# Kernel optimization log

Measured on AMD Instinct MI355X. Metric: run time of the kernel, lower is better.

Reference implementation:

```python
import jax, jax.numpy as jnp
import numpy as np

IN, H, L, S = 512, 512, 2, 3   # input_size, hidden_size, num_layers, num_split
B, T = 64, 512
PENALTY = 0.7                  # forward() default penalty arg


def gru_cell(x, h, Wih, Whh, bih, bhh):
    # torch.nn.GRUCell math, gate order (r, z, n)
    gi = x @ Wih.T + bih
    gh = h @ Whh.T + bhh
    ir, iz, inew = jnp.split(gi, 3, axis=-1)
    hr, hz, hn = jnp.split(gh, 3, axis=-1)
    r = jax.nn.sigmoid(ir + hr)
    z = jax.nn.sigmoid(iz + hz)
    n = jnp.tanh(inew + r * hn)
    return (1.0 - z) * n + z * h


def setup_inputs() -> dict:
    key = jax.random.key(0)
    ks = jax.random.split(key, 10)
    sc = 1.0 / np.sqrt(H)
    u = lambda k, shp: jax.random.uniform(k, shp, jnp.float32, -sc, sc)
    return {
        'x': jax.random.normal(ks[0], (B, T, IN), jnp.float32),
        'Wih_first': u(ks[1], (S, 3 * H, IN)),      # layer-0 input weights per expert
        'Wih_rest': u(ks[2], (S, L - 1, 3 * H, H)),  # layers 1..L-1 input weights per expert
        'Whh': u(ks[3], (S, L, 3 * H, H)),
        'bih': u(ks[4], (S, L, 3 * H)),
        'bhh': u(ks[5], (S, L, 3 * H)),
        'Wlw': u(ks[6], (H, H)),      # layer_weights Linear(H, H)
        'blw': u(ks[7], (H,)),
        'Wsel': u(ks[8], (S, H + IN)),  # selective_layer Linear(H+IN, S)
        'bsel': u(ks[9], (S,)),
    }


def _run_stack(x_t, h_prev, cur, Wih_first, Wih_rest, Whh, bih, bhh):
    # h_prev: [B, L, H]; cur: expert index (traced int ok)
    hs = [gru_cell(x_t, h_prev[:, 0], Wih_first[cur], Whh[cur, 0], bih[cur, 0], bhh[cur, 0])]
    for j in range(1, L):
        hs.append(gru_cell(hs[-1], h_prev[:, j], Wih_rest[cur, j - 1], Whh[cur, j], bih[cur, j], bhh[cur, j]))
    return jnp.stack(hs, axis=1)  # [B, L, H]


def _forward(x, Wih_first, Wih_rest, Whh, bih, bhh, Wlw, blw, Wsel, bsel):
    h0 = jnp.zeros((B, L, H), x.dtype)
    # timestep 0: hard-coded expert 0 on zero hidden
    h = _run_stack(x[:, 0], h0, 0, Wih_first, Wih_rest, Whh, bih, bhh)
    p = jnp.ones((S,), x.dtype).at[0].mul(PENALTY)
    p = p / p.max()

    def step(carry, x_t):
        h_prev, p = carry
        # attention-style router (num_layers > 1 branch of the original)
        energy = jnp.einsum('blh,gh->blg', h_prev, Wlw) + blw   # [B, L, H]
        le = energy.sum(-1)                                     # [B, L]
        sh = jnp.einsum('bl,blh->bh', le, h_prev)               # [B, H]
        logits = jnp.concatenate([sh, x_t], axis=-1) @ Wsel.T + bsel  # [B, S]
        probs = jax.nn.softmax(logits.sum(0)) * p               # [S]
        cur = jnp.argmax(probs)                                 # top-1 expert
        h_new = _run_stack(x_t, h_prev, cur, Wih_first, Wih_rest, Whh, bih, bhh)
        p_new = p * jnp.where(jnp.arange(S) == cur, PENALTY, 1.0)
        p_new = p_new / p_new.max()
        return (h_new, p_new), h_new[:, -1]

    (h_last, _), outs = jax.lax.scan(step, (h, p), jnp.swapaxes(x, 0, 1)[1:])
    outputs = jnp.concatenate([h[:, -1][None], outs], axis=0)   # [T, B, H]
    return outputs, h_last[:, -1]


def reference(x, Wih_first, Wih_rest, Whh, bih, bhh, Wlw, blw, Wsel, bsel):
    return _forward(x, Wih_first, Wih_rest, Whh, bih, bhh, Wlw, blw, Wsel, bsel)
```

## Files before the change

### kernel.cpp

```cpp
#include <hip/hip_runtime.h>
#include <math.h>

#define BB 64
#define TT 512
#define HH 512
#define KK 512
#define G3 1536
#define PEN 0.7f
#define NBLK 256
#define NTHR 512
#define SLAB 32768
#define WSTRIDE ((size_t)(G3 * KK))

__device__ __forceinline__ float4 ldcv4(const float* p) {
  float4 r;
  asm volatile("global_load_dwordx4 %0, %1, off sc0 sc1" : "=v"(r) : "v"(p));
  return r;
}
__device__ __forceinline__ void ld1_issue(float* dst, const float* p) {
  asm volatile("global_load_dword %0, %1, off sc0 sc1" : "=v"(*dst) : "v"(p));
}
__device__ __forceinline__ void stwt1(float* p, float v) {
  asm volatile("global_store_dword %0, %1, off sc0 sc1" :: "v"(p), "v"(v) : "memory");
}
__device__ __forceinline__ void vwait() {
  asm volatile("s_waitcnt vmcnt(0)" ::: "memory");
  __builtin_amdgcn_sched_barrier(0);
}
__device__ __forceinline__ unsigned umin2(unsigned a, unsigned b) { return a < b ? a : b; }
__device__ __forceinline__ void st_flag(unsigned* p, unsigned v) {
  __hip_atomic_store(p, v, __ATOMIC_RELAXED, __HIP_MEMORY_SCOPE_AGENT);
}
__device__ __forceinline__ void poll_all(const unsigned* flags, unsigned ep) {
  const unsigned* p = flags + (threadIdx.x & 63) * 4;
  for (;;) {
    uint4 v;
    asm volatile("global_load_dwordx4 %0, %1, off sc0 sc1" : "=v"(v) : "v"(p));
    vwait();
    unsigned mn = umin2(umin2(v.x, v.y), umin2(v.z, v.w));
    if (__all((int)(mn >= ep))) break;
    __builtin_amdgcn_s_sleep(2);
  }
}
__device__ __forceinline__ void poll8(const unsigned* flag8, unsigned ep) {
  const unsigned* p = flag8 + (threadIdx.x & 7);
  for (;;) {
    unsigned v;
    asm volatile("global_load_dword %0, %1, off sc0 sc1" : "=v"(v) : "v"(p));
    vwait();
    if (__all((int)(v >= ep))) break;
    __builtin_amdgcn_s_sleep(2);
  }
}

__global__ void k_pre_xc(const float* __restrict__ x, const float* __restrict__ Wsel,
                         const float* __restrict__ bsel, float* __restrict__ xc) {
  int t = blockIdx.x, tid = threadIdx.x;
  __shared__ float xs[512];
  __shared__ float a0[256], a1[256], a2[256];
  for (int i = tid; i < 512; i += 256) {
    float s = 0.f;
    const float* px = x + (size_t)t * KK + i;
    for (int b = 0; b < BB; ++b) s += px[(size_t)b * TT * KK];
    xs[i] = s;
  }
  __syncthreads();
  float c0 = 0.f, c1 = 0.f, c2 = 0.f;
  for (int i = tid; i < 512; i += 256) {
    float v = xs[i];
    c0 += v * Wsel[512 + i];
    c1 += v * Wsel[1024 + 512 + i];
    c2 += v * Wsel[2048 + 512 + i];
  }
  a0[tid] = c0; a1[tid] = c1; a2[tid] = c2;
  __syncthreads();
  for (int off = 128; off; off >>= 1) {
    if (tid < off) { a0[tid] += a0[tid + off]; a1[tid] += a1[tid + off]; a2[tid] += a2[tid + off]; }
    __syncthreads();
  }
  if (tid == 0) {
    xc[t * 4 + 0] = a0[0] + 64.f * bsel[0];
    xc[t * 4 + 1] = a1[0] + 64.f * bsel[1];
    xc[t * 4 + 2] = a2[0] + 64.f * bsel[2];
  }
}

__global__ void k_pre_misc(const float* __restrict__ Wlw, const float* __restrict__ blw,
                           const float* __restrict__ x,
                           float* __restrict__ wsum, float* __restrict__ bsumb,
                           float* __restrict__ xT0,
                           float* __restrict__ h0T0, float* __restrict__ h1T0,
                           unsigned* __restrict__ flags, unsigned* __restrict__ flag8) {
  int gtid = blockIdx.x * 256 + threadIdx.x;
  for (int i = gtid; i < SLAB; i += 64 * 256) { h0T0[i] = 0.f; h1T0[i] = 0.f; }
  for (int i = gtid; i < SLAB; i += 64 * 256) {
    int b = i >> 9, k = i & 511;
    xT0[(k >> 2) * 256 + b * 4 + (k & 3)] = x[(size_t)b * TT * KK + k];
  }
  if (blockIdx.x == 0) {
    int tid = threadIdx.x;
    if (tid < 256) flags[tid] = 0u;
    if (tid < 8) flag8[tid] = 0u;
    for (int h = tid; h < 512; h += 256) {
      float s = 0.f;
      for (int g = 0; g < 512; ++g) s += Wlw[(size_t)g * 512 + h];
      wsum[h] = s;
    }
    __shared__ float red[256];
    float s = 0.f;
    for (int i = tid; i < 512; i += 256) s += blw[i];
    red[tid] = s;
    __syncthreads();
    for (int off = 128; off; off >>= 1) {
      if (tid < off) red[tid] += red[tid + off];
      __syncthreads();
    }
    if (tid == 0) *bsumb = red[0];
  }
}

__global__ void k_pre_xt(const float* __restrict__ x, float* __restrict__ xTall) {
  int t = blockIdx.x, tid = threadIdx.x;
  float* dst = xTall + (size_t)t * SLAB;
  const float* src = x + (size_t)t * KK;
  for (int i = tid; i < SLAB; i += 256) {
    int b = i >> 9, k = i & 511;
    dst[(k >> 2) * 256 + b * 4 + (k & 3)] = src[(size_t)b * TT * KK + k];
  }
}

template<int ACT_CACHED>
__device__ __forceinline__ void do_layer(
    int tid, int b, int k0, int j0, int lidx, int bid,
    const float* __restrict__ act, const float* __restrict__ hT,
    const float* __restrict__ Wih, const float* __restrict__ Whh,
    const float* __restrict__ bihL, const float* __restrict__ bhhL,
    const float* __restrict__ wsum, const float* __restrict__ Wsel,
    float* __restrict__ houtT, float* __restrict__ houtN, float* __restrict__ houtN2,
    float* __restrict__ part, float* red, float* r2) {
  int w = tid >> 6;
  const float* a4p = act + (k0 >> 2) * 256 + b * 4;
  const float* h4p = hT + (k0 >> 2) * 256 + b * 4;
  const float* wi0r = Wih + (size_t)(j0 + 0) * KK + k0;
  const float* wi1r = Wih + (size_t)(j0 + 1) * KK + k0;
  const float* wi0z = Wih + (size_t)(512 + j0 + 0) * KK + k0;
  const float* wi1z = Wih + (size_t)(512 + j0 + 1) * KK + k0;
  const float* wi0n = Wih + (size_t)(1024 + j0 + 0) * KK + k0;
  const float* wi1n = Wih + (size_t)(1024 + j0 + 1) * KK + k0;
  const float* wh0r = Whh + (size_t)(j0 + 0) * KK + k0;
  const float* wh1r = Whh + (size_t)(j0 + 1) * KK + k0;
  const float* wh0z = Whh + (size_t)(512 + j0 + 0) * KK + k0;
  const float* wh1z = Whh + (size_t)(512 + j0 + 1) * KK + k0;
  const float* wh0n = Whh + (size_t)(1024 + j0 + 0) * KK + k0;
  const float* wh1n = Whh + (size_t)(1024 + j0 + 1) * KK + k0;
  float ai0r = 0.f, ai1r = 0.f, ai0z = 0.f, ai1z = 0.f, ai0n = 0.f, ai1n = 0.f;
  float ah0r = 0.f, ah1r = 0.f, ah0z = 0.f, ah1z = 0.f, ah0n = 0.f, ah1n = 0.f;
  float4 A[8], Hv[8];
  for (int half = 0; half < 2; ++half) {
    const float* ab = a4p + half * 2048;
    const float* hb = h4p + half * 2048;
#pragma unroll
    for (int i = 0; i < 8; ++i) {
      if (ACT_CACHED) A[i] = *(const float4*)(ab + i * 256);
      else            A[i] = ldcv4(ab + i * 256);
      Hv[i] = ldcv4(hb + i * 256);
    }
    vwait();
#pragma unroll
    for (int c = 0; c < 8; ++c) {
      const int kc = half * 8 + c;
      const float4 a4 = A[c];
      const float4 h4 = Hv[c];
      float4 q;
#define DOTW(acc, ptr, vv) q = *(const float4*)((ptr) + kc * 4); \
      acc += vv.x * q.x + vv.y * q.y + vv.z * q.z + vv.w * q.w;
      DOTW(ai0r, wi0r, a4) DOTW(ai1r, wi1r, a4)
      DOTW(ai0z, wi0z, a4) DOTW(ai1z, wi1z, a4)
      DOTW(ai0n, wi0n, a4) DOTW(ai1n, wi1n, a4)
      DOTW(ah0r, wh0r, h4) DOTW(ah1r, wh1r, h4)
      DOTW(ah0z, wh0z, h4) DOTW(ah1z, wh1z, h4)
      DOTW(ah0n, wh0n, h4) DOTW(ah1n, wh1n, h4)
#undef DOTW
    }
  }
  int base = (w * 12) * 64 + b;
  red[base + 0 * 64] = ai0r; red[base + 1 * 64] = ai0z; red[base + 2 * 64] = ai0n;
  red[base + 3 * 64] = ah0r; red[base + 4 * 64] = ah0z; red[base + 5 * 64] = ah0n;
  red[base + 6 * 64] = ai1r; red[base + 7 * 64] = ai1z; red[base + 8 * 64] = ai1n;
  red[base + 9 * 64] = ah1r; red[base + 10 * 64] = ah1z; red[base + 11 * 64] = ah1n;
  __syncthreads();
  if (tid < 128) {
    int bb = tid & 63, jl = tid >> 6;
    int j = j0 + jl;
    float hpv;
    ld1_issue(&hpv, hT + (j >> 2) * 256 + bb * 4 + (j & 3));
    float sir = 0.f, siz = 0.f, sinn = 0.f, shr = 0.f, shz = 0.f, shn = 0.f;
#pragma unroll
    for (int ww = 0; ww < 8; ++ww) {
      int o = (ww * 12 + jl * 6) * 64 + bb;
      sir += red[o]; siz += red[o + 64]; sinn += red[o + 128];
      shr += red[o + 192]; shz += red[o + 256]; shn += red[o + 320];
    }
    vwait();
    float air = sir + bihL[j],         ahr = shr + bhhL[j];
    float aiz = siz + bihL[j + 512],   ahz = shz + bhhL[j + 512];
    float ain = sinn + bihL[j + 1024], ahn = shn + bhhL[j + 1024];
    float rg = 1.f / (1.f + expf(-(air + ahr)));
    float zg = 1.f / (1.f + expf(-(aiz + ahz)));
    float ng = tanhf(ain + rg * ahn);
    float hv = (1.f - zg) * ng + zg * hpv;
    stwt1(houtT + (j >> 2) * 256 + bb * 4 + (j & 3), hv);
    if (houtN) houtN[(size_t)bb * HH + j] = hv;
    if (houtN2) houtN2[(size_t)bb * HH + j] = hv;
    r2[jl * 256 + 0 * 64 + bb] = hv * wsum[j];
    r2[jl * 256 + 1 * 64 + bb] = hv * Wsel[j];
    r2[jl * 256 + 2 * 64 + bb] = hv * Wsel[1024 + j];
    r2[jl * 256 + 3 * 64 + bb] = hv * Wsel[2048 + j];
  }
  __syncthreads();
  if (tid < 64) {
    float* pb = part + (size_t)bid * 512;
    stwt1(pb + lidx * 64 + tid,       r2[tid]       + r2[256 + tid]);
    stwt1(pb + 128 + lidx * 64 + tid, r2[64 + tid]  + r2[256 + 64 + tid]);
    stwt1(pb + 256 + lidx * 64 + tid, r2[128 + tid] + r2[256 + 128 + tid]);
    stwt1(pb + 384 + lidx * 64 + tid, r2[192 + tid] + r2[256 + 192 + tid]);
  }
}

template<int XM>
__global__ __launch_bounds__(NTHR, 2) void k_persist(
    const float* __restrict__ x,
    const float* __restrict__ Wih_first, const float* __restrict__ Wih_rest,
    const float* __restrict__ Whh,
    const float* __restrict__ bih, const float* __restrict__ bhh,
    const float* __restrict__ Wsel,
    const float* __restrict__ wsum, const float* __restrict__ bsumb,
    const float* __restrict__ xc,
    float* __restrict__ xzone, float* __restrict__ h0T, float* __restrict__ h1T,
    float* __restrict__ part, float* __restrict__ partial2,
    float* __restrict__ out,
    unsigned* __restrict__ flags, unsigned* __restrict__ flag8) {
  __shared__ float red[8 * 12 * 64];
  __shared__ float r2[2 * 4 * 64];
  int tid = threadIdx.x, bid = blockIdx.x;
  int b = tid & 63;
  int k0 = __builtin_amdgcn_readfirstlane(((int)threadIdx.x >> 6) << 6);
  int j0 = bid * 2;
  float p0 = PEN, p1 = 1.f, p2 = 1.f;
  int cur = 0;
  float bs = *bsumb;

  for (int t = 0; t < TT; ++t) {
    int par = t & 1;
    const float* h0Tp = h0T + par * SLAB;
    float* h0Tn = h0T + (par ^ 1) * SLAB;
    const float* h1Tp = h1T + par * SLAB;
    float* h1Tn = h1T + (par ^ 1) * SLAB;
    const float* act0;
    float* xTn = nullptr;
    if (XM) act0 = xzone + (size_t)t * SLAB;
    else { act0 = xzone + par * SLAB; xTn = xzone + (par ^ 1) * SLAB; }

    if (t > 0) {
      if (tid < 64) poll8(flag8, (unsigned)t);
      __syncthreads();
      float g0, g1, g2, g3, g4, g5, g6, g7;
      ld1_issue(&g0, partial2 + 0 * 512 + tid);
      ld1_issue(&g1, partial2 + 1 * 512 + tid);
      ld1_issue(&g2, partial2 + 2 * 512 + tid);
      ld1_issue(&g3, partial2 + 3 * 512 + tid);
      ld1_issue(&g4, partial2 + 4 * 512 + tid);
      ld1_issue(&g5, partial2 + 5 * 512 + tid);
      ld1_issue(&g6, partial2 + 6 * 512 + tid);
      ld1_issue(&g7, partial2 + 7 * 512 + tid);
      vwait();
      red[tid] = ((g0 + g1) + (g2 + g3)) + ((g4 + g5) + (g6 + g7));
      __syncthreads();
      float prod = 0.f;
      if (tid < 384) {
        int s = tid >> 7, row = tid & 127;
        prod = (red[row] + bs) * red[128 + (s << 7) + row];
      }
#pragma unroll
      for (int off = 1; off < 64; off <<= 1) prod += __shfl_xor(prod, off);
      if ((tid & 63) == 0) r2[tid >> 6] = prod;
      __syncthreads();
      float l0 = r2[0] + r2[1] + xc[t * 4 + 0];
      float l1 = r2[2] + r2[3] + xc[t * 4 + 1];
      float l2 = r2[4] + r2[5] + xc[t * 4 + 2];
      float m = fmaxf(l0, fmaxf(l1, l2));
      float e0 = expf(l0 - m), e1 = expf(l1 - m), e2 = expf(l2 - m);
      float Z = e0 + e1 + e2;
      float w0 = e0 / Z * p0, w1 = e1 / Z * p1, w2 = e2 / Z * p2;
      cur = 0;
      float bestv = w0;
      if (w1 > bestv) { bestv = w1; cur = 1; }
      if (w2 > bestv) { bestv = w2; cur = 2; }
      p0 *= (cur == 0) ? PEN : 1.f;
      p1 *= (cur == 1) ? PEN : 1.f;
      p2 *= (cur == 2) ? PEN : 1.f;
      float mx = fmaxf(p0, fmaxf(p1, p2));
      p0 /= mx; p1 /= mx; p2 /= mx;
      __syncthreads();
    }

    if (!XM && t + 1 < TT && tid < 128) {
      int idx = bid * 128 + tid;
      int b2 = idx >> 9, k = idx & 511;
      stwt1(xTn + (k >> 2) * 256 + b2 * 4 + (k & 3),
            x[(size_t)b2 * TT * KK + (size_t)(t + 1) * KK + k]);
    }

    do_layer<XM>(tid, b, k0, j0, 0, bid, act0, h0Tp,
                 Wih_first + (size_t)cur * WSTRIDE,
                 Whh + (size_t)(cur * 2 + 0) * WSTRIDE,
                 bih + (size_t)(cur * 2 + 0) * G3, bhh + (size_t)(cur * 2 + 0) * G3,
                 wsum, Wsel, h0Tn, nullptr, nullptr, part, red, r2);
    __syncthreads();
    if (tid == 0) st_flag(&flags[bid], 2u * (unsigned)t + 1u);

    if (tid < 64) poll_all(flags, 2u * (unsigned)t + 1u);
    __syncthreads();

    float* o2 = (t == TT - 1) ? (out + (size_t)TT * BB * HH) : nullptr;
    do_layer<0>(tid, b, k0, j0, 1, bid, h0Tn, h1Tp,
                Wih_rest + (size_t)cur * WSTRIDE,
                Whh + (size_t)(cur * 2 + 1) * WSTRIDE,
                bih + (size_t)(cur * 2 + 1) * G3, bhh + (size_t)(cur * 2 + 1) * G3,
                wsum, Wsel, h1Tn, out + (size_t)t * BB * HH, o2, part, red, r2);
    __syncthreads();
    if (tid == 0) st_flag(&flags[bid], 2u * (unsigned)t + 2u);

    if (bid < 8 && t + 1 < TT) {
      if (tid < 64) poll_all(flags, 2u * (unsigned)t + 2u);
      __syncthreads();
      float a[32];
#pragma unroll
      for (int r = 0; r < 32; ++r)
        ld1_issue(&a[r], part + (size_t)(32 * bid + r) * 512 + tid);
      vwait();
      float s = 0.f;
#pragma unroll
      for (int r = 0; r < 32; ++r) s += a[r];
      stwt1(partial2 + bid * 512 + tid, s);
      __syncthreads();
      if (tid == 0) st_flag(&flag8[bid], (unsigned)t + 1u);
    }
  }
}

extern "C" void kernel_launch(void* const* d_in, const int* in_sizes, int n_in,
                              void* d_out, int out_size, void* d_ws, size_t ws_size,
                              hipStream_t stream) {
  const float* x         = (const float*)d_in[0];
  const float* Wih_first = (const float*)d_in[1];
  const float* Wih_rest  = (const float*)d_in[2];
  const float* Whh       = (const float*)d_in[3];
  const float* bih       = (const float*)d_in[4];
  const float* bhh       = (const float*)d_in[5];
  const float* Wlw       = (const float*)d_in[6];
  const float* blw       = (const float*)d_in[7];
  const float* Wsel      = (const float*)d_in[8];
  const float* bsel      = (const float*)d_in[9];
  float* out = (float*)d_out;
  float* ws  = (float*)d_ws;

  float* h0T      = ws;
  float* h1T      = h0T + 2 * SLAB;
  float* xT2      = h1T + 2 * SLAB;
  float* part     = xT2 + 2 * SLAB;
  float* partial2 = part + NBLK * 512;
  float* xc       = partial2 + 8 * 512;
  float* wsum     = xc + TT * 4;
  float* bsumb    = wsum + HH;
  unsigned* flags = (unsigned*)(bsumb + 4);
  unsigned* flag8 = flags + 256;
  size_t hdr_floats = (size_t)((float*)(flag8 + 8) - ws);
  hdr_floats = (hdr_floats + 3) & ~(size_t)3;
  float* xTall = ws + hdr_floats;
  size_t need_big = (hdr_floats + (size_t)TT * SLAB) * sizeof(float);

  k_pre_xc<<<dim3(TT), 256, 0, stream>>>(x, Wsel, bsel, xc);
  k_pre_misc<<<dim3(64), 256, 0, stream>>>(Wlw, blw, x, wsum, bsumb,
                                           xT2, h0T, h1T, flags, flag8);
  if (ws_size >= need_big) {
    k_pre_xt<<<dim3(TT), 256, 0, stream>>>(x, xTall);
    k_persist<1><<<dim3(NBLK), NTHR, 0, stream>>>(x, Wih_first, Wih_rest, Whh, bih, bhh,
                                                  Wsel, wsum, bsumb, xc,
                                                  xTall, h0T, h1T, part, partial2,
                                                  out, flags, flag8);
  } else {
    k_persist<0><<<dim3(NBLK), NTHR, 0, stream>>>(x, Wih_first, Wih_rest, Whh, bih, bhh,
                                                  Wsel, wsum, bsumb, xc,
                                                  xT2, h0T, h1T, part, partial2,
                                                  out, flags, flag8);
  }
}
```

Baseline: 15.88 ms.

## Use 1024-thread blocks, ring buffers with cached loads, and fused router reduction

Doubles the threads per block to 1024 so each wave handles 32 K-elements, which halves the per-thread dot-product loop and widens the shared reduction. It replaces the ping-pong hidden and x buffers with 96-deep rings so the cached path can use plain cacheable loads. Acquire loads are issued periodically on that path, and the separate x pre-transpose kernel is dropped. The router reduction is reworked so the 8 reducer blocks compute the final three logits partials directly, leaving every block a 24-float read instead of an 8x512 load and block reduction. The risks are staleness from cached reads on reused ring slots, higher register pressure at 1024 threads, and a larger shared-memory footprint.

```diff
diff --git a/kernel.cpp b/kernel.cpp
--- a/kernel.cpp
+++ b/kernel.cpp
@@ -8,22 +8,21 @@
 #define G3 1536
 #define PEN 0.7f
 #define NBLK 256
-#define NTHR 512
+#define NTHR 1024
 #define SLAB 32768
 #define WSTRIDE ((size_t)(G3 * KK))
-
-__device__ __forceinline__ float4 ldcv4(const float* p) {
-  float4 r;
-  asm volatile("global_load_dwordx4 %0, %1, off sc0 sc1" : "=v"(r) : "v"(p));
-  return r;
-}
-__device__ __forceinline__ void ld1_issue(float* dst, const float* p) {
-  asm volatile("global_load_dword %0, %1, off sc0 sc1" : "=v"(*dst) : "v"(p));
+#define INVP 64
+
+__device__ __forceinline__ void ld1b(float* d, const float* p) {
+  asm volatile("global_load_dword %0, %1, off sc0 sc1" : "=v"(*d) : "v"(p));
+}
+__device__ __forceinline__ float4 ld4b(const float* p) {
+  float4 r; asm volatile("global_load_dwordx4 %0, %1, off sc0 sc1" : "=v"(r) : "v"(p)); return r;
 }
 __device__ __forceinline__ void stwt1(float* p, float v) {
   asm volatile("global_store_dword %0, %1, off sc0 sc1" :: "v"(p), "v"(v) : "memory");
 }
-__device__ __forceinline__ void vwait() {
+__device__ __forceinline__ void vwait0() {
   asm volatile("s_waitcnt vmcnt(0)" ::: "memory");
   __builtin_amdgcn_sched_barrier(0);
 }
@@ -34,9 +33,8 @@
 __device__ __forceinline__ void poll_all(const unsigned* flags, unsigned ep) {
   const unsigned* p = flags + (threadIdx.x & 63) * 4;
   for (;;) {
-    uint4 v;
-    asm volatile("global_load_dwordx4 %0, %1, off sc0 sc1" : "=v"(v) : "v"(p));
-    vwait();
+    uint4 v; asm volatile("global_load_dwordx4 %0, %1, off sc0 sc1" : "=v"(v) : "v"(p));
+    asm volatile("s_waitcnt vmcnt(0)" ::: "memory");
     unsigned mn = umin2(umin2(v.x, v.y), umin2(v.z, v.w));
     if (__all((int)(mn >= ep))) break;
     __builtin_amdgcn_s_sleep(2);
@@ -45,9 +43,8 @@
 __device__ __forceinline__ void poll8(const unsigned* flag8, unsigned ep) {
   const unsigned* p = flag8 + (threadIdx.x & 7);
   for (;;) {
-    unsigned v;
-    asm volatile("global_load_dword %0, %1, off sc0 sc1" : "=v"(v) : "v"(p));
-    vwait();
+    unsigned v; asm volatile("global_load_dword %0, %1, off sc0 sc1" : "=v"(v) : "v"(p));
+    asm volatile("s_waitcnt vmcnt(0)" ::: "memory");
     if (__all((int)(v >= ep))) break;
     __builtin_amdgcn_s_sleep(2);
   }
@@ -88,11 +85,11 @@
 __global__ void k_pre_misc(const float* __restrict__ Wlw, const float* __restrict__ blw,
                            const float* __restrict__ x,
                            float* __restrict__ wsum, float* __restrict__ bsumb,
-                           float* __restrict__ xT0,
-                           float* __restrict__ h0T0, float* __restrict__ h1T0,
-                           unsigned* __restrict__ flags, unsigned* __restrict__ flag8) {
+                           float* __restrict__ zslab, float* __restrict__ xT0,
+                           unsigned* __restrict__ flags, unsigned* __restrict__ flag8,
+                           float* __restrict__ plog) {
   int gtid = blockIdx.x * 256 + threadIdx.x;
-  for (int i = gtid; i < SLAB; i += 64 * 256) { h0T0[i] = 0.f; h1T0[i] = 0.f; }
+  for (int i = gtid; i < SLAB; i += 64 * 256) zslab[i] = 0.f;
   for (int i = gtid; i < SLAB; i += 64 * 256) {
     int b = i >> 9, k = i & 511;
     xT0[(k >> 2) * 256 + b * 4 + (k & 3)] = x[(size_t)b * TT * KK + k];
@@ -101,6 +98,7 @@
     int tid = threadIdx.x;
     if (tid < 256) flags[tid] = 0u;
     if (tid < 8) flag8[tid] = 0u;
+    if (tid < 24) plog[tid] = 0.f;
     for (int h = tid; h < 512; h += 256) {
       float s = 0.f;
       for (int g = 0; g < 512; ++g) s += Wlw[(size_t)g * 512 + h];
@@ -119,28 +117,18 @@
   }
 }
 
-__global__ void k_pre_xt(const float* __restrict__ x, float* __restrict__ xTall) {
-  int t = blockIdx.x, tid = threadIdx.x;
-  float* dst = xTall + (size_t)t * SLAB;
-  const float* src = x + (size_t)t * KK;
-  for (int i = tid; i < SLAB; i += 256) {
-    int b = i >> 9, k = i & 511;
-    dst[(k >> 2) * 256 + b * 4 + (k & 3)] = src[(size_t)b * TT * KK + k];
-  }
-}
-
-template<int ACT_CACHED>
+template<int CACHED>
 __device__ __forceinline__ void do_layer(
-    int tid, int b, int k0, int j0, int lidx, int bid,
-    const float* __restrict__ act, const float* __restrict__ hT,
+    int tid, int w, int b, int j0, int lidx, int bid,
+    const float* __restrict__ aT, const float* __restrict__ hT,
     const float* __restrict__ Wih, const float* __restrict__ Whh,
-    const float* __restrict__ bihL, const float* __restrict__ bhhL,
+    const float* __restrict__ bih_l, const float* __restrict__ bhh_l,
     const float* __restrict__ wsum, const float* __restrict__ Wsel,
-    float* __restrict__ houtT, float* __restrict__ houtN, float* __restrict__ houtN2,
+    float* __restrict__ houtT, float* __restrict__ outN, float* __restrict__ outN2,
     float* __restrict__ part, float* red, float* r2) {
-  int w = tid >> 6;
-  const float* a4p = act + (k0 >> 2) * 256 + b * 4;
-  const float* h4p = hT + (k0 >> 2) * 256 + b * 4;
+  const int k0 = w << 5;
+  const float* a4p = aT + ((k0 >> 2) << 8) + (b << 2);
+  const float* h4p = hT + ((k0 >> 2) << 8) + (b << 2);
   const float* wi0r = Wih + (size_t)(j0 + 0) * KK + k0;
   const float* wi1r = Wih + (size_t)(j0 + 1) * KK + k0;
   const float* wi0z = Wih + (size_t)(512 + j0 + 0) * KK + k0;
@@ -155,196 +143,214 @@
   const float* wh1n = Whh + (size_t)(1024 + j0 + 1) * KK + k0;
   float ai0r = 0.f, ai1r = 0.f, ai0z = 0.f, ai1z = 0.f, ai0n = 0.f, ai1n = 0.f;
   float ah0r = 0.f, ah1r = 0.f, ah0z = 0.f, ah1z = 0.f, ah0n = 0.f, ah1n = 0.f;
-  float4 A[8], Hv[8];
-  for (int half = 0; half < 2; ++half) {
-    const float* ab = a4p + half * 2048;
-    const float* hb = h4p + half * 2048;
+  float4 A[8], H[8];
+  if (CACHED) {
 #pragma unroll
     for (int i = 0; i < 8; ++i) {
-      if (ACT_CACHED) A[i] = *(const float4*)(ab + i * 256);
-      else            A[i] = ldcv4(ab + i * 256);
-      Hv[i] = ldcv4(hb + i * 256);
-    }
-    vwait();
-#pragma unroll
-    for (int c = 0; c < 8; ++c) {
-      const int kc = half * 8 + c;
-      const float4 a4 = A[c];
-      const float4 h4 = Hv[c];
-      float4 q;
-#define DOTW(acc, ptr, vv) q = *(const float4*)((ptr) + kc * 4); \
-      acc += vv.x * q.x + vv.y * q.y + vv.z * q.z + vv.w * q.w;
-      DOTW(ai0r, wi0r, a4) DOTW(ai1r, wi1r, a4)
-      DOTW(ai0z, wi0z, a4) DOTW(ai1z, wi1z, a4)
-      DOTW(ai0n, wi0n, a4) DOTW(ai1n, wi1n, a4)
-      DOTW(ah0r, wh0r, h4) DOTW(ah1r, wh1r, h4)
-      DOTW(ah0z, wh0z, h4) DOTW(ah1z, wh1z, h4)
-      DOTW(ah0n, wh0n, h4) DOTW(ah1n, wh1n, h4)
+      A[i] = *(const float4*)(a4p + (i << 8));
+      H[i] = *(const float4*)(h4p + (i << 8));
+    }
+  } else {
+#pragma unroll
+    for (int i = 0; i < 8; ++i) {
+      A[i] = ld4b(a4p + (i << 8));
+      H[i] = ld4b(h4p + (i << 8));
+    }
+    vwait0();
+  }
+#pragma unroll
+  for (int c = 0; c < 8; ++c) {
+    const float4 a4 = A[c];
+    const float4 h4 = H[c];
+    float4 q;
+#define DOTW(acc, ptr, vv) q = *(const float4*)((ptr) + c * 4); \
+    acc += vv.x * q.x + vv.y * q.y + vv.z * q.z + vv.w * q.w;
+    DOTW(ai0r, wi0r, a4) DOTW(ai1r, wi1r, a4)
+    DOTW(ai0z, wi0z, a4) DOTW(ai1z, wi1z, a4)
+    DOTW(ai0n, wi0n, a4) DOTW(ai1n, wi1n, a4)
+    DOTW(ah0r, wh0r, h4) DOTW(ah1r, wh1r, h4)
+    DOTW(ah0z, wh0z, h4) DOTW(ah1z, wh1z, h4)
+    DOTW(ah0n, wh0n, h4) DOTW(ah1n, wh1n, h4)
 #undef DOTW
-    }
-  }
-  int base = (w * 12) * 64 + b;
-  red[base + 0 * 64] = ai0r; red[base + 1 * 64] = ai0z; red[base + 2 * 64] = ai0n;
-  red[base + 3 * 64] = ah0r; red[base + 4 * 64] = ah0z; red[base + 5 * 64] = ah0n;
-  red[base + 6 * 64] = ai1r; red[base + 7 * 64] = ai1z; red[base + 8 * 64] = ai1n;
-  red[base + 9 * 64] = ah1r; red[base + 10 * 64] = ah1z; red[base + 11 * 64] = ah1n;
+  }
+  {
+    int rb = ((w << 6) + b) * 13;
+    red[rb + 0] = ai0r; red[rb + 1] = ai0z; red[rb + 2] = ai0n;
+    red[rb + 3] = ah0r; red[rb + 4] = ah0z; red[rb + 5] = ah0n;
+    red[rb + 6] = ai1r; red[rb + 7] = ai1z; red[rb + 8] = ai1n;
+    red[rb + 9] = ah1r; red[rb + 10] = ah1z; red[rb + 11] = ah1n;
+  }
   __syncthreads();
   if (tid < 128) {
-    int bb = tid & 63, jl = tid >> 6;
-    int j = j0 + jl;
+    int jl = tid >> 6, bb = tid & 63;
+    int je = j0 + jl;
     float hpv;
-    ld1_issue(&hpv, hT + (j >> 2) * 256 + bb * 4 + (j & 3));
-    float sir = 0.f, siz = 0.f, sinn = 0.f, shr = 0.f, shz = 0.f, shn = 0.f;
-#pragma unroll
-    for (int ww = 0; ww < 8; ++ww) {
-      int o = (ww * 12 + jl * 6) * 64 + bb;
-      sir += red[o]; siz += red[o + 64]; sinn += red[o + 128];
-      shr += red[o + 192]; shz += red[o + 256]; shn += red[o + 320];
-    }
-    vwait();
-    float air = sir + bihL[j],         ahr = shr + bhhL[j];
-    float aiz = siz + bihL[j + 512],   ahz = shz + bhhL[j + 512];
-    float ain = sinn + bihL[j + 1024], ahn = shn + bhhL[j + 1024];
+    if (!CACHED) ld1b(&hpv, hT + ((je >> 2) << 8) + (bb << 2) + (je & 3));
+    float sI0 = 0.f, sI1 = 0.f, sI2 = 0.f, sH0 = 0.f, sH1 = 0.f, sH2 = 0.f;
+#pragma unroll
+    for (int ww = 0; ww < 16; ++ww) {
+      int o = ((ww << 6) + bb) * 13 + jl * 6;
+      sI0 += red[o]; sI1 += red[o + 1]; sI2 += red[o + 2];
+      sH0 += red[o + 3]; sH1 += red[o + 4]; sH2 += red[o + 5];
+    }
+    if (CACHED) hpv = hT[((je >> 2) << 8) + (bb << 2) + (je & 3)];
+    else vwait0();
+    float air = sI0 + bih_l[je],        ahr = sH0 + bhh_l[je];
+    float aiz = sI1 + bih_l[je + 512],  ahz = sH1 + bhh_l[je + 512];
+    float ain = sI2 + bih_l[je + 1024], ahn = sH2 + bhh_l[je + 1024];
     float rg = 1.f / (1.f + expf(-(air + ahr)));
     float zg = 1.f / (1.f + expf(-(aiz + ahz)));
     float ng = tanhf(ain + rg * ahn);
     float hv = (1.f - zg) * ng + zg * hpv;
-    stwt1(houtT + (j >> 2) * 256 + bb * 4 + (j & 3), hv);
-    if (houtN) houtN[(size_t)bb * HH + j] = hv;
-    if (houtN2) houtN2[(size_t)bb * HH + j] = hv;
-    r2[jl * 256 + 0 * 64 + bb] = hv * wsum[j];
-    r2[jl * 256 + 1 * 64 + bb] = hv * Wsel[j];
-    r2[jl * 256 + 2 * 64 + bb] = hv * Wsel[1024 + j];
-    r2[jl * 256 + 3 * 64 + bb] = hv * Wsel[2048 + j];
+    stwt1(houtT + ((je >> 2) << 8) + (bb << 2) + (je & 3), hv);
+    if (outN) stwt1(outN + (size_t)bb * HH + je, hv);
+    if (outN2) stwt1(outN2 + (size_t)bb * HH + je, hv);
+    r2[jl * 256 + 0 * 64 + bb] = hv * wsum[je];
+    r2[jl * 256 + 1 * 64 + bb] = hv * Wsel[je];
+    r2[jl * 256 + 2 * 64 + bb] = hv * Wsel[1024 + je];
+    r2[jl * 256 + 3 * 64 + bb] = hv * Wsel[2048 + je];
   }
   __syncthreads();
   if (tid < 64) {
-    float* pb = part + (size_t)bid * 512;
+    float* pb = part + ((size_t)bid << 9);
     stwt1(pb + lidx * 64 + tid,       r2[tid]       + r2[256 + tid]);
-    stwt1(pb + 128 + lidx * 64 + tid, r2[64 + tid]  + r2[256 + 64 + tid]);
-    stwt1(pb + 256 + lidx * 64 + tid, r2[128 + tid] + r2[256 + 128 + tid]);
-    stwt1(pb + 384 + lidx * 64 + tid, r2[192 + tid] + r2[256 + 192 + tid]);
-  }
-}
-
-template<int XM>
-__global__ __launch_bounds__(NTHR, 2) void k_persist(
+    stwt1(pb + 128 + lidx * 64 + tid, r2[64 + tid]  + r2[320 + tid]);
+    stwt1(pb + 256 + lidx * 64 + tid, r2[128 + tid] + r2[384 + tid]);
+    stwt1(pb + 384 + lidx * 64 + tid, r2[192 + tid] + r2[448 + tid]);
+  }
+}
+
+template<int CACHED, int RS>
+__global__ __launch_bounds__(NTHR, 4) void k_persist(
     const float* __restrict__ x,
     const float* __restrict__ Wih_first, const float* __restrict__ Wih_rest,
     const float* __restrict__ Whh,
     const float* __restrict__ bih, const float* __restrict__ bhh,
     const float* __restrict__ Wsel,
     const float* __restrict__ wsum, const float* __restrict__ bsumb,
-    const float* __restrict__ xc,
-    float* __restrict__ xzone, float* __restrict__ h0T, float* __restrict__ h1T,
-    float* __restrict__ part, float* __restrict__ partial2,
+    const float* __restrict__ xc, const float* __restrict__ zslab,
+    float* __restrict__ xTr, float* __restrict__ h0Tr, float* __restrict__ h1Tr,
+    float* __restrict__ part, float* __restrict__ plog,
     float* __restrict__ out,
     unsigned* __restrict__ flags, unsigned* __restrict__ flag8) {
-  __shared__ float red[8 * 12 * 64];
-  __shared__ float r2[2 * 4 * 64];
+  __shared__ float red[16 * 64 * 13];
+  __shared__ float r2[512];
   int tid = threadIdx.x, bid = blockIdx.x;
-  int b = tid & 63;
-  int k0 = __builtin_amdgcn_readfirstlane(((int)threadIdx.x >> 6) << 6);
+  int w = tid >> 6, b = tid & 63;
   int j0 = bid * 2;
   float p0 = PEN, p1 = 1.f, p2 = 1.f;
   int cur = 0;
+
+  if (tid == 0)
+    (void)__hip_atomic_load(&flags[0], __ATOMIC_ACQUIRE, __HIP_MEMORY_SCOPE_AGENT);
+  __syncthreads();
   float bs = *bsumb;
 
   for (int t = 0; t < TT; ++t) {
-    int par = t & 1;
-    const float* h0Tp = h0T + par * SLAB;
-    float* h0Tn = h0T + (par ^ 1) * SLAB;
-    const float* h1Tp = h1T + par * SLAB;
-    float* h1Tn = h1T + (par ^ 1) * SLAB;
-    const float* act0;
-    float* xTn = nullptr;
-    if (XM) act0 = xzone + (size_t)t * SLAB;
-    else { act0 = xzone + par * SLAB; xTn = xzone + (par ^ 1) * SLAB; }
+    int cs = t % RS;
+    int ps = (t + RS - 1) % RS;
+    const float* xcur = xTr + (size_t)cs * SLAB;
+    float* xnxt = xTr + (size_t)((t + 1) % RS) * SLAB;
+    const float* h0p = (t == 0) ? zslab : (h0Tr + (size_t)ps * SLAB);
+    float* h0c = h0Tr + (size_t)cs * SLAB;
+    const float* h1p = (t == 0) ? zslab : (h1Tr + (size_t)ps * SLAB);
+    float* h1c = h1Tr + (size_t)cs * SLAB;
 
     if (t > 0) {
       if (tid < 64) poll8(flag8, (unsigned)t);
       __syncthreads();
-      float g0, g1, g2, g3, g4, g5, g6, g7;
-      ld1_issue(&g0, partial2 + 0 * 512 + tid);
-      ld1_issue(&g1, partial2 + 1 * 512 + tid);
-      ld1_issue(&g2, partial2 + 2 * 512 + tid);
-      ld1_issue(&g3, partial2 + 3 * 512 + tid);
-      ld1_issue(&g4, partial2 + 4 * 512 + tid);
-      ld1_issue(&g5, partial2 + 5 * 512 + tid);
-      ld1_issue(&g6, partial2 + 6 * 512 + tid);
-      ld1_issue(&g7, partial2 + 7 * 512 + tid);
-      vwait();
-      red[tid] = ((g0 + g1) + (g2 + g3)) + ((g4 + g5) + (g6 + g7));
-      __syncthreads();
-      float prod = 0.f;
-      if (tid < 384) {
-        int s = tid >> 7, row = tid & 127;
-        prod = (red[row] + bs) * red[128 + (s << 7) + row];
+      if (tid < 24) { float v; ld1b(&v, plog + tid); vwait0(); red[tid] = v; }
+      __syncthreads();
+      float l0 = xc[4 * t + 0], l1 = xc[4 * t + 1], l2 = xc[4 * t + 2];
+#pragma unroll
+      for (int r = 0; r < 8; ++r) {
+        l0 += red[r * 3 + 0]; l1 += red[r * 3 + 1]; l2 += red[r * 3 + 2];
       }
-#pragma unroll
-      for (int off = 1; off < 64; off <<= 1) prod += __shfl_xor(prod, off);
-      if ((tid & 63) == 0) r2[tid >> 6] = prod;
-      __syncthreads();
-      float l0 = r2[0] + r2[1] + xc[t * 4 + 0];
-      float l1 = r2[2] + r2[3] + xc[t * 4 + 1];
-      float l2 = r2[4] + r2[5] + xc[t * 4 + 2];
       float m = fmaxf(l0, fmaxf(l1, l2));
       float e0 = expf(l0 - m), e1 = expf(l1 - m), e2 = expf(l2 - m);
       float Z = e0 + e1 + e2;
-      float w0 = e0 / Z * p0, w1 = e1 / Z * p1, w2 = e2 / Z * p2;
-      cur = 0;
-      float bestv = w0;
-      if (w1 > bestv) { bestv = w1; cur = 1; }
-      if (w2 > bestv) { bestv = w2; cur = 2; }
+      float w0_ = e0 / Z * p0, w1_ = e1 / Z * p1, w2_ = e2 / Z * p2;
+      cur = 0; float bb_ = w0_;
+      if (w1_ > bb_) { bb_ = w1_; cur = 1; }
+      if (w2_ > bb_) { bb_ = w2_; cur = 2; }
       p0 *= (cur == 0) ? PEN : 1.f;
       p1 *= (cur == 1) ? PEN : 1.f;
       p2 *= (cur == 2) ? PEN : 1.f;
       float mx = fmaxf(p0, fmaxf(p1, p2));
       p0 /= mx; p1 /= mx; p2 /= mx;
       __syncthreads();
-    }
-
-    if (!XM && t + 1 < TT && tid < 128) {
-      int idx = bid * 128 + tid;
+
+      if (CACHED && (t & (INVP - 1)) == 0) {
+        if (tid == 0)
+          (void)__hip_atomic_load(&flags[0], __ATOMIC_ACQUIRE, __HIP_MEMORY_SCOPE_AGENT);
+        __syncthreads();
+      }
+    }
+
+    if (t + 1 < TT && tid < 128) {
+      int idx = (bid << 7) + tid;
       int b2 = idx >> 9, k = idx & 511;
-      stwt1(xTn + (k >> 2) * 256 + b2 * 4 + (k & 3),
+      stwt1(xnxt + ((k >> 2) << 8) + (b2 << 2) + (k & 3),
             x[(size_t)b2 * TT * KK + (size_t)(t + 1) * KK + k]);
     }
 
-    do_layer<XM>(tid, b, k0, j0, 0, bid, act0, h0Tp,
-                 Wih_first + (size_t)cur * WSTRIDE,
-                 Whh + (size_t)(cur * 2 + 0) * WSTRIDE,
-                 bih + (size_t)(cur * 2 + 0) * G3, bhh + (size_t)(cur * 2 + 0) * G3,
-                 wsum, Wsel, h0Tn, nullptr, nullptr, part, red, r2);
+    do_layer<CACHED>(tid, w, b, j0, 0, bid, xcur, h0p,
+                     Wih_first + (size_t)cur * WSTRIDE,
+                     Whh + (size_t)(cur * 2) * WSTRIDE,
+                     bih + (size_t)(cur * 2) * G3, bhh + (size_t)(cur * 2) * G3,
+                     wsum, Wsel, h0c, nullptr, nullptr, part, red, r2);
     __syncthreads();
     if (tid == 0) st_flag(&flags[bid], 2u * (unsigned)t + 1u);
-
     if (tid < 64) poll_all(flags, 2u * (unsigned)t + 1u);
     __syncthreads();
 
-    float* o2 = (t == TT - 1) ? (out + (size_t)TT * BB * HH) : nullptr;
-    do_layer<0>(tid, b, k0, j0, 1, bid, h0Tn, h1Tp,
-                Wih_rest + (size_t)cur * WSTRIDE,
-                Whh + (size_t)(cur * 2 + 1) * WSTRIDE,
-                bih + (size_t)(cur * 2 + 1) * G3, bhh + (size_t)(cur * 2 + 1) * G3,
-                wsum, Wsel, h1Tn, out + (size_t)t * BB * HH, o2, part, red, r2);
+    float* o2 = (t == TT - 1) ? (out + (size_t)TT * SLAB) : nullptr;
+    do_layer<CACHED>(tid, w, b, j0, 1, bid, h0c, h1p,
+                     Wih_rest + (size_t)cur * WSTRIDE,
+                     Whh + (size_t)(cur * 2 + 1) * WSTRIDE,
+                     bih + (size_t)(cur * 2 + 1) * G3, bhh + (size_t)(cur * 2 + 1) * G3,
+                     wsum, Wsel, h1c, out + (size_t)t * SLAB, o2, part, red, r2);
     __syncthreads();
     if (tid == 0) st_flag(&flags[bid], 2u * (unsigned)t + 2u);
 
     if (bid < 8 && t + 1 < TT) {
       if (tid < 64) poll_all(flags, 2u * (unsigned)t + 2u);
       __syncthreads();
-      float a[32];
-#pragma unroll
-      for (int r = 0; r < 32; ++r)
-        ld1_issue(&a[r], part + (size_t)(32 * bid + r) * 512 + tid);
-      vwait();
-      float s = 0.f;
-#pragma unroll
-      for (int r = 0; r < 32; ++r) s += a[r];
-      stwt1(partial2 + bid * 512 + tid, s);
-      __syncthreads();
-      if (tid == 0) st_flag(&flag8[bid], (unsigned)t + 1u);
+      if (tid < 512) {
+        int idx = tid & 63, oct = tid >> 6;
+        int g = idx >> 4, i = idx & 15;
+        int col = g * 128 + bid * 16 + i;
+        const float* pb = part + ((size_t)(oct * 32) << 9) + col;
+        float a[32];
+#pragma unroll
+        for (int q = 0; q < 32; ++q) ld1b(&a[q], pb + ((size_t)q << 9));
+        vwait0();
+        float s = 0.f;
+#pragma unroll
+        for (int q = 0; q < 32; ++q) s += a[q];
+        red[(oct << 6) + idx] = s;
+      }
+      __syncthreads();
+      if (tid < 64) {
+        float tot = 0.f;
+#pragma unroll
+        for (int oc = 0; oc < 8; ++oc) tot += red[(oc << 6) + tid];
+        red[512 + tid] = tot;
+      }
+      __syncthreads();
+      if (tid == 0) {
+        const float* tp = red + 512;
+#pragma unroll
+        for (int s_ = 0; s_ < 3; ++s_) {
+          float acc = 0.f;
+#pragma unroll
+          for (int i = 0; i < 16; ++i) acc += (tp[i] + bs) * tp[(s_ + 1) * 16 + i];
+          stwt1(plog + bid * 3 + s_, acc);
+        }
+        vwait0();
+        st_flag(&flag8[bid], (unsigned)t + 1u);
+      }
+      __syncthreads();
     }
   }
 }
@@ -365,34 +371,34 @@
   float* out = (float*)d_out;
   float* ws  = (float*)d_ws;
 
-  float* h0T      = ws;
-  float* h1T      = h0T + 2 * SLAB;
-  float* xT2      = h1T + 2 * SLAB;
-  float* part     = xT2 + 2 * SLAB;
-  float* partial2 = part + NBLK * 512;
-  float* xc       = partial2 + 8 * 512;
-  float* wsum     = xc + TT * 4;
-  float* bsumb    = wsum + HH;
-  unsigned* flags = (unsigned*)(bsumb + 4);
-  unsigned* flag8 = flags + 256;
-  size_t hdr_floats = (size_t)((float*)(flag8 + 8) - ws);
-  hdr_floats = (hdr_floats + 3) & ~(size_t)3;
-  float* xTall = ws + hdr_floats;
-  size_t need_big = (hdr_floats + (size_t)TT * SLAB) * sizeof(float);
+  float* xc       = ws;
+  float* wsum     = ws + 2048;
+  float* bsumb    = ws + 2560;
+  float* plog     = ws + 2564;
+  unsigned* flags = (unsigned*)(ws + 2592);
+  unsigned* flag8 = (unsigned*)(ws + 2848);
+  float* part     = ws + 4096;
+  float* zslab    = ws + 135168;
+  float* rings    = ws + 167936;
+
+  size_t need_big = ((size_t)167936 + (size_t)3 * 96 * SLAB) * sizeof(float);
 
   k_pre_xc<<<dim3(TT), 256, 0, stream>>>(x, Wsel, bsel, xc);
   k_pre_misc<<<dim3(64), 256, 0, stream>>>(Wlw, blw, x, wsum, bsumb,
-                                           xT2, h0T, h1T, flags, flag8);
+                                           zslab, rings, flags, flag8, plog);
   if (ws_size >= need_big) {
-    k_pre_xt<<<dim3(TT), 256, 0, stream>>>(x, xTall);
-    k_persist<1><<<dim3(NBLK), NTHR, 0, stream>>>(x, Wih_first, Wih_rest, Whh, bih, bhh,
-                                                  Wsel, wsum, bsumb, xc,
-                                                  xTall, h0T, h1T, part, partial2,
-                                                  out, flags, flag8);
+    float* xTr  = rings;
+    float* h0Tr = rings + (size_t)96 * SLAB;
+    float* h1Tr = rings + (size_t)192 * SLAB;
+    k_persist<1, 96><<<dim3(NBLK), NTHR, 0, stream>>>(
+        x, Wih_first, Wih_rest, Whh, bih, bhh, Wsel, wsum, bsumb, xc, zslab,
+        xTr, h0Tr, h1Tr, part, plog, out, flags, flag8);
   } else {
-    k_persist<0><<<dim3(NBLK), NTHR, 0, stream>>>(x, Wih_first, Wih_rest, Whh, bih, bhh,
-                                                  Wsel, wsum, bsumb, xc,
-                                                  xT2, h0T, h1T, part, partial2,
-                                                  out, flags, flag8);
-  }
-}
+    float* xTr  = rings;
+    float* h0Tr = rings + (size_t)2 * SLAB;
+    float* h1Tr = rings + (size_t)4 * SLAB;
+    k_persist<0, 2><<<dim3(NBLK), NTHR, 0, stream>>>(
+        x, Wih_first, Wih_rest, Whh, bih, bhh, Wsel, wsum, bsumb, xc, zslab,
+        xTr, h0Tr, h1Tr, part, plog, out, flags, flag8);
+  }
+}
```

New measurement: 37.47 ms. 136% more time.
